# Optimization experiments

Hardware: AMD Instinct MI355X
Metric: run time of the kernel (lower is better)

## Reference

```python
import jax, jax.numpy as jnp
import numpy as np

N, B, DIN, H, D, E = 20000, 2, 128, 4, 64, 320000
NEG_SLOPE = 0.2


def _leaky(x):
    return jnp.where(x >= 0, x, NEG_SLOPE * x)


def setup_inputs() -> dict:
    key = jax.random.key(0)
    k1, k2, k3, k4, k5, k6 = jax.random.split(key, 6)
    feat = jax.random.normal(k1, (N, B, DIN), dtype=jnp.float32)
    # fc weight, xavier-ish scale; stored as (Din, H*D) so projection is feat @ W
    W = jax.random.normal(k2, (DIN, H * D), dtype=jnp.float32) * (1.0 / np.sqrt(DIN))
    attn_l = jax.random.normal(k3, (H, D), dtype=jnp.float32) * 0.1
    attn_r = jax.random.normal(k4, (H, D), dtype=jnp.float32) * 0.1
    src = jax.random.randint(k5, (E,), 0, N, dtype=jnp.int32)
    dst = jax.random.randint(k6, (E,), 0, N, dtype=jnp.int32)
    return {"feat": feat, "W": W, "attn_l": attn_l, "attn_r": attn_r, "src": src, "dst": dst}


def reference(feat, W, attn_l, attn_r, src, dst):
    # feat: (N,B,Din) -> projected features (N,B,H,D)
    ft = (feat @ W).reshape(N, B, H, D)
    # per-node attention logits (N,B,H)
    el = jnp.einsum('nbhd,hd->nbh', ft, attn_l)
    er = jnp.einsum('nbhd,hd->nbh', ft, attn_r)
    # edge logits: u_add_v then LeakyReLU, shape (E,B,H)
    e = _leaky(el[src] + er[dst])
    # edge softmax normalized per destination node (numerically stable)
    emax = jax.ops.segment_max(e, dst, num_segments=N)
    emax = jnp.where(jnp.isfinite(emax), emax, 0.0)  # nodes with no in-edges
    ex = jnp.exp(e - emax[dst])
    denom = jax.ops.segment_sum(ex, dst, num_segments=N)
    a = ex / denom[dst]                               # (E,B,H); denom>0 for every edge's dst
    # u_mul_e messages and sum-aggregation by dst
    m = ft[src] * a[..., None]                        # (E,B,H,D)
    rst = jax.ops.segment_sum(m, dst, num_segments=N)  # (N,B,H,D)
    # module sets self.activation = leaky_relu unconditionally
    return _leaky(rst)
```

## Files before the change

kernel.cpp:

```cpp
#include <hip/hip_runtime.h>
#include <hip/hip_bf16.h>
#include <math.h>


typedef unsigned short ushort;
typedef __attribute__((ext_vector_type(8))) unsigned short ushort8;
typedef __attribute__((ext_vector_type(8))) short short8v;
typedef __attribute__((ext_vector_type(4))) float f32x4;

constexpr int DIN = 128;
constexpr int B   = 2;
constexpr int H   = 4;
constexpr int D   = 64;
constexpr int HD  = H * D;
constexpr int BHD = B * HD;
constexpr int NCOL = 272;
constexpr int PREP_ELEMS  = NCOL * DIN;
constexpr int PREP_BLOCKS = (PREP_ELEMS + 255) / 256;
constexpr int SXS = 72;

__device__ __forceinline__ float leaky(float x) { return x >= 0.f ? x : 0.2f * x; }

__device__ __forceinline__ ushort f2bf(float f) {
    return __builtin_bit_cast(ushort, __float2bfloat16(f));
}
__device__ __forceinline__ float bf2f(ushort v) {
    return __uint_as_float(((unsigned int)v) << 16);
}

__global__ __launch_bounds__(256) void hist_prep_kernel(
    const int* __restrict__ dst, int* __restrict__ deg, int E,
    const float* __restrict__ W, const float* __restrict__ attn_l,
    const float* __restrict__ attn_r, ushort* __restrict__ WT, int histBlocks)
{
    const int t = threadIdx.x;
    const int b = blockIdx.x;
    if (b < histBlocks) {
        int e4 = (b * 256 + t) * 4;
        if (e4 + 3 < E) {
            int4 dd = *(const int4*)(dst + e4);
            atomicAdd(&deg[dd.x], 1); atomicAdd(&deg[dd.y], 1);
            atomicAdd(&deg[dd.z], 1); atomicAdd(&deg[dd.w], 1);
        } else {
            for (int e = e4; e < E; ++e) atomicAdd(&deg[dst[e]], 1);
        }
        return;
    }
    int id = (b - histBlocks) * 256 + t;
    if (id >= PREP_ELEMS) return;
    int c = id >> 7, k = id & 127;
    float v;
    if (c < 256) {
        v = W[k * HD + c];
    } else if (c < 264) {
        int j = c - 256, h = j & 3;
        const float* av = (j < 4 ? attn_l : attn_r) + h * D;
        const float* wp = W + k * HD + h * D;
        float s = 0.f;
        for (int d = 0; d < D; ++d) s = fmaf(wp[d], av[d], s);
        v = s;
    } else {
        v = 0.f;
    }
    WT[c * DIN + k] = f2bf(v);
}

__device__ void scan_body(const int* __restrict__ deg, int* __restrict__ offs,
                          int* __restrict__ cursor, int n)
{
    __shared__ int wcarry[4];
    const int t = threadIdx.x;
    const int lane = t & 63;
    const int wid = t >> 6;
    int carry = 0;
    const int nstripes = (n + 1023) >> 10;
    for (int s = 0; s < nstripes; ++s) {
        const int base = (s << 10) + t * 4;
        int4 d = make_int4(0, 0, 0, 0);
        if (base + 3 < n) {
            d = *(const int4*)(deg + base);
        } else {
            if (base     < n) d.x = deg[base];
            if (base + 1 < n) d.y = deg[base + 1];
            if (base + 2 < n) d.z = deg[base + 2];
        }
        const int sum4 = (d.x + d.y) + (d.z + d.w);
        int inc = sum4;
#pragma unroll
        for (int o = 1; o < 64; o <<= 1) {
            int v = __shfl_up(inc, o, 64);
            if (lane >= o) inc += v;
        }
        if (lane == 63) wcarry[wid] = inc;
        __syncthreads();
        int wpre = carry;
#pragma unroll
        for (int k = 0; k < 4; ++k) if (k < wid) wpre += wcarry[k];
        const int e0 = wpre + inc - sum4;
        int4 ov;
        ov.x = e0; ov.y = e0 + d.x; ov.z = ov.y + d.y; ov.w = ov.z + d.z;
        if (base + 3 < n) {
            *(int4*)(offs + base) = ov;
            *(int4*)(cursor + base) = ov;
        } else {
            if (base     < n) { offs[base]     = ov.x; cursor[base]     = ov.x; }
            if (base + 1 < n) { offs[base + 1] = ov.y; cursor[base + 1] = ov.y; }
            if (base + 2 < n) { offs[base + 2] = ov.z; cursor[base + 2] = ov.z; }
        }
        carry += (wcarry[0] + wcarry[1]) + (wcarry[2] + wcarry[3]);
        __syncthreads();
    }
    if (t == 0) offs[n] = carry;
}

__global__ __launch_bounds__(256) void proj_scan_kernel(
    const float* __restrict__ feat, const ushort* __restrict__ WT,
    ushort* __restrict__ ftb, float* __restrict__ el, float* __restrict__ er,
    const int* __restrict__ deg, int* __restrict__ offs, int* __restrict__ cursor,
    int N, int nTiles)
{
    if ((int)blockIdx.x >= nTiles) {
        scan_body(deg, offs, cursor, N);
        return;
    }
    __shared__ ushort sxp[4][2][16][SXS];
    const int t = threadIdx.x;
    const int w = t >> 6;
    const int lane = t & 63;
    const int lr = lane & 15;
    const int lk = lane >> 4;

    short8v bfrag[4][4];
#pragma unroll
    for (int ct = 0; ct < 4; ++ct) {
        const int col = w * 64 + ct * 16 + lr;
#pragma unroll
        for (int ks = 0; ks < 4; ++ks)
            bfrag[ct][ks] = *(const short8v*)&WT[col * DIN + ks * 32 + lk * 8];
    }
    short8v efrag[4];
#pragma unroll
    for (int ks = 0; ks < 4; ++ks)
        efrag[ks] = *(const short8v*)&WT[(256 + lr) * DIN + ks * 32 + lk * 8];

    const int row0 = blockIdx.x * 64;
    const int rrow = lane >> 2;
    const int seg  = lane & 3;

    auto loadA = [&](int rt, short8v aout[4]) {
        const float* fp = feat + (size_t)(row0 + rt * 16 + lr) * DIN + lk * 8;
#pragma unroll
        for (int ks = 0; ks < 4; ++ks) {
            f32x4 x0 = *(const f32x4*)(fp + ks * 32);
            f32x4 x1 = *(const f32x4*)(fp + ks * 32 + 4);
            short8v v;
            v[0] = (short)f2bf(x0[0]); v[1] = (short)f2bf(x0[1]);
            v[2] = (short)f2bf(x0[2]); v[3] = (short)f2bf(x0[3]);
            v[4] = (short)f2bf(x1[0]); v[5] = (short)f2bf(x1[1]);
            v[6] = (short)f2bf(x1[2]); v[7] = (short)f2bf(x1[3]);
            aout[ks] = v;
        }
    };

    short8v aP[4], aN[4];
    loadA(0, aP);

#pragma unroll
    for (int rt = 0; rt < 4; ++rt) {
        if (rt < 3) loadA(rt + 1, aN);

        f32x4 acc[4] = {{0.f,0.f,0.f,0.f},{0.f,0.f,0.f,0.f},{0.f,0.f,0.f,0.f},{0.f,0.f,0.f,0.f}};
#pragma unroll
        for (int ct = 0; ct < 4; ++ct)
#pragma unroll
            for (int ks = 0; ks < 4; ++ks)
                acc[ct] = __builtin_amdgcn_mfma_f32_16x16x32_bf16(aP[ks], bfrag[ct][ks], acc[ct], 0, 0, 0);

        ushort (* __restrict__ sw)[SXS] = sxp[w][rt & 1];
#pragma unroll
        for (int ct = 0; ct < 4; ++ct)
#pragma unroll
            for (int r = 0; r < 4; ++r)
                sw[lk * 4 + r][ct * 16 + lr] = f2bf(acc[ct][r]);
        __builtin_amdgcn_wave_barrier();
        ushort8 o0 = *(const ushort8*)&sw[rrow][seg * 16];
        ushort8 o1 = *(const ushort8*)&sw[rrow][seg * 16 + 8];
        ushort* gp = ftb + (size_t)(row0 + rt * 16 + rrow) * HD + w * 64 + seg * 16;
        *(ushort8*)gp = o0;
        *(ushort8*)(gp + 8) = o1;

        if (rt == w) {
            f32x4 acce = {0.f, 0.f, 0.f, 0.f};
#pragma unroll
            for (int ks = 0; ks < 4; ++ks)
                acce = __builtin_amdgcn_mfma_f32_16x16x32_bf16(aP[ks], efrag[ks], acce, 0, 0, 0);
#pragma unroll
            for (int r = 0; r < 4; ++r) {
                const int row = row0 + rt * 16 + lk * 4 + r;
                if (lr < 4)       el[row * 4 + lr]       = acce[r];
                else if (lr < 8)  er[row * 4 + (lr - 4)] = acce[r];
            }
        }

#pragma unroll
        for (int ks = 0; ks < 4; ++ks) aP[ks] = aN[ks];
    }
}

__global__ __launch_bounds__(256) void scatter_kernel(
    const int* __restrict__ dst, const int* __restrict__ src,
    int* __restrict__ cursor, int* __restrict__ esrc, int E)
{
    int e4 = (blockIdx.x * 256 + threadIdx.x) * 4;
    if (e4 + 3 < E) {
        int4 dd = *(const int4*)(dst + e4);
        int4 ss = *(const int4*)(src + e4);
        int p0 = atomicAdd(&cursor[dd.x], 1); esrc[p0] = ss.x;
        int p1 = atomicAdd(&cursor[dd.y], 1); esrc[p1] = ss.y;
        int p2 = atomicAdd(&cursor[dd.z], 1); esrc[p2] = ss.z;
        int p3 = atomicAdd(&cursor[dd.w], 1); esrc[p3] = ss.w;
    } else {
        for (int e = e4; e < E; ++e) {
            int pos = atomicAdd(&cursor[dst[e]], 1);
            esrc[pos] = src[e];
        }
    }
}

__global__ __launch_bounds__(256) void agg_kernel(
    const ushort* __restrict__ ftb, const float* __restrict__ el,
    const float* __restrict__ er, const int* __restrict__ offs,
    const int* __restrict__ esrc, float* __restrict__ out, int N)
{
    const int t = threadIdx.x;
    const int n = blockIdx.x * 4 + (t >> 6);
    if (n >= N) return;
    const int lane = t & 63;
    const int bh = lane >> 3;
    const int beg = offs[n];
    const int end = offs[n + 1];

    const float erd = er[n * 8 + bh];
    const ushort8* __restrict__ ftv = (const ushort8*)ftb;

    float acc[8];
#pragma unroll
    for (int j = 0; j < 8; ++j) acc[j] = 0.f;
    float dsum = 0.f;

    int i = beg;
    for (; i + 15 < end; i += 16) {
        int s[16];
#pragma unroll
        for (int u = 0; u < 16; ++u) s[u] = esrc[i + u];
        float w[16];
#pragma unroll
        for (int u = 0; u < 16; ++u) w[u] = __expf(leaky(el[s[u] * 8 + bh] + erd));
        ushort8 v[16];
#pragma unroll
        for (int u = 0; u < 16; ++u) v[u] = ftv[s[u] * 64 + lane];
#pragma unroll
        for (int u = 0; u < 16; ++u) dsum += w[u];
#pragma unroll
        for (int j = 0; j < 8; ++j) {
            float a = acc[j];
#pragma unroll
            for (int u = 0; u < 16; ++u) a = fmaf(w[u], bf2f(v[u][j]), a);
            acc[j] = a;
        }
    }
    for (; i + 3 < end; i += 4) {
        int s[4];
#pragma unroll
        for (int u = 0; u < 4; ++u) s[u] = esrc[i + u];
        float w[4];
#pragma unroll
        for (int u = 0; u < 4; ++u) w[u] = __expf(leaky(el[s[u] * 8 + bh] + erd));
        ushort8 v[4];
#pragma unroll
        for (int u = 0; u < 4; ++u) v[u] = ftv[s[u] * 64 + lane];
#pragma unroll
        for (int u = 0; u < 4; ++u) dsum += w[u];
#pragma unroll
        for (int j = 0; j < 8; ++j) {
            float a = acc[j];
#pragma unroll
            for (int u = 0; u < 4; ++u) a = fmaf(w[u], bf2f(v[u][j]), a);
            acc[j] = a;
        }
    }
    for (; i < end; ++i) {
        int s0 = esrc[i];
        float w0 = __expf(leaky(el[s0 * 8 + bh] + erd));
        ushort8 v0 = ftv[s0 * 64 + lane];
        dsum += w0;
#pragma unroll
        for (int j = 0; j < 8; ++j) acc[j] = fmaf(w0, bf2f(v0[j]), acc[j]);
    }

    const float sc = (end > beg) ? (1.f / dsum) : 0.f;
    float4 o0, o1;
    o0.x = leaky(acc[0] * sc); o0.y = leaky(acc[1] * sc);
    o0.z = leaky(acc[2] * sc); o0.w = leaky(acc[3] * sc);
    o1.x = leaky(acc[4] * sc); o1.y = leaky(acc[5] * sc);
    o1.z = leaky(acc[6] * sc); o1.w = leaky(acc[7] * sc);
    float* op = out + (size_t)n * BHD + lane * 8;
    *(float4*)op = o0;
    *(float4*)(op + 4) = o1;
}

extern "C" void kernel_launch(void* const* d_in, const int* in_sizes, int n_in,
                              void* d_out, int out_size, void* d_ws, size_t ws_size,
                              hipStream_t stream)
{
    const float* feat   = (const float*)d_in[0];
    const float* W      = (const float*)d_in[1];
    const float* attn_l = (const float*)d_in[2];
    const float* attn_r = (const float*)d_in[3];
    const int*   src    = (const int*)d_in[4];
    const int*   dst    = (const int*)d_in[5];
    float* out = (float*)d_out;

    const int N = in_sizes[0] / (B * DIN);
    const int E = in_sizes[4];
    const int R = N * B;
    const int nTiles = R / 64;
    const int histBlocks = (E / 4 + 255) / 256;
    const int edgeBlocks = histBlocks;

    auto align_up = [](size_t x) { return (x + 255) & ~(size_t)255; };
    size_t off = 0;
    char* base = (char*)d_ws;
    ushort* ftb = (ushort*)(base + off); off += align_up((size_t)R * HD * sizeof(ushort));
    float* el   = (float*)(base + off); off += align_up((size_t)R * H * sizeof(float));
    float* er   = (float*)(base + off); off += align_up((size_t)R * H * sizeof(float));
    ushort* WT  = (ushort*)(base + off); off += align_up((size_t)NCOL * DIN * sizeof(ushort));
    int* deg    = (int*)(base + off); off += align_up((size_t)N * sizeof(int));
    int* offs   = (int*)(base + off); off += align_up((size_t)(N + 1) * sizeof(int));
    int* cursor = (int*)(base + off); off += align_up((size_t)N * sizeof(int));
    int* esrc   = (int*)(base + off); off += align_up((size_t)E * sizeof(int));
    (void)ws_size; (void)n_in; (void)out_size;

    hipMemsetAsync(deg, 0, (size_t)N * sizeof(int), stream);

    hist_prep_kernel<<<histBlocks + PREP_BLOCKS, 256, 0, stream>>>(
        dst, deg, E, W, attn_l, attn_r, WT, histBlocks);
    proj_scan_kernel<<<nTiles + 1, 256, 0, stream>>>(
        feat, WT, ftb, el, er, deg, offs, cursor, N, nTiles);
    scatter_kernel<<<edgeBlocks, 256, 0, stream>>>(dst, src, cursor, esrc, E);
    agg_kernel<<<(N + 3) / 4, 256, 0, stream>>>(ftb, el, er, offs, esrc, out, N);
}
```

Baseline: 128.7 us.

## Store projected features per (batch,head) plane and split aggregation by head across blocks

The projection kernel now writes bf16 features as 8 separate (batch,head) planes of N×64 instead of interleaved per node. The aggregation kernel launches 8× more blocks, each handling one (batch,head) slice. Within a wave, 8 lane groups each process a different edge, and the partial sums are combined with xor shuffles. The goal is better locality for the gathers from each plane and more edge-level parallelism per wave, so gather latency is hidden better for low-degree nodes. The cost is that esrc and el are reread once per head, the shuffle reduction adds work, and only one lane group writes the output.

```diff
diff --git a/kernel.cpp b/kernel.cpp
--- a/kernel.cpp
+++ b/kernel.cpp
@@ -115,7 +115,7 @@
 
 __global__ __launch_bounds__(256) void proj_scan_kernel(
     const float* __restrict__ feat, const ushort* __restrict__ WT,
-    ushort* __restrict__ ftb, float* __restrict__ el, float* __restrict__ er,
+    ushort* __restrict__ ftt, float* __restrict__ el, float* __restrict__ er,
     const int* __restrict__ deg, int* __restrict__ offs, int* __restrict__ cursor,
     int N, int nTiles)
 {
@@ -185,7 +185,10 @@
         __builtin_amdgcn_wave_barrier();
         ushort8 o0 = *(const ushort8*)&sw[rrow][seg * 16];
         ushort8 o1 = *(const ushort8*)&sw[rrow][seg * 16 + 8];
-        ushort* gp = ftb + (size_t)(row0 + rt * 16 + rrow) * HD + w * 64 + seg * 16;
+        const int row = row0 + rt * 16 + rrow;
+        const int nn = row >> 1;
+        const int bb = row & 1;
+        ushort* gp = ftt + ((size_t)(bb * 4 + w) * N + nn) * 64 + seg * 16;
         *(ushort8*)gp = o0;
         *(ushort8*)(gp + 8) = o1;
 
@@ -196,9 +199,9 @@
                 acce = __builtin_amdgcn_mfma_f32_16x16x32_bf16(aP[ks], efrag[ks], acce, 0, 0, 0);
 #pragma unroll
             for (int r = 0; r < 4; ++r) {
-                const int row = row0 + rt * 16 + lk * 4 + r;
-                if (lr < 4)       el[row * 4 + lr]       = acce[r];
-                else if (lr < 8)  er[row * 4 + (lr - 4)] = acce[r];
+                const int row2 = row0 + rt * 16 + lk * 4 + r;
+                if (lr < 4)       el[row2 * 4 + lr]       = acce[r];
+                else if (lr < 8)  er[row2 * 4 + (lr - 4)] = acce[r];
             }
         }
 
@@ -228,85 +231,69 @@
 }
 
 __global__ __launch_bounds__(256) void agg_kernel(
-    const ushort* __restrict__ ftb, const float* __restrict__ el,
+    const ushort* __restrict__ ftt, const float* __restrict__ el,
     const float* __restrict__ er, const int* __restrict__ offs,
     const int* __restrict__ esrc, float* __restrict__ out, int N)
 {
     const int t = threadIdx.x;
-    const int n = blockIdx.x * 4 + (t >> 6);
+    const int bh = blockIdx.x & 7;
+    const int n  = (blockIdx.x >> 3) * 4 + (t >> 6);
     if (n >= N) return;
     const int lane = t & 63;
-    const int bh = lane >> 3;
+    const int g  = lane >> 3;
+    const int d8 = lane & 7;
     const int beg = offs[n];
     const int end = offs[n + 1];
-
     const float erd = er[n * 8 + bh];
-    const ushort8* __restrict__ ftv = (const ushort8*)ftb;
+    const ushort8* __restrict__ fv = (const ushort8*)(ftt + (size_t)bh * N * 64);
 
     float acc[8];
 #pragma unroll
     for (int j = 0; j < 8; ++j) acc[j] = 0.f;
     float dsum = 0.f;
 
-    int i = beg;
-    for (; i + 15 < end; i += 16) {
-        int s[16];
-#pragma unroll
-        for (int u = 0; u < 16; ++u) s[u] = esrc[i + u];
-        float w[16];
-#pragma unroll
-        for (int u = 0; u < 16; ++u) w[u] = __expf(leaky(el[s[u] * 8 + bh] + erd));
-        ushort8 v[16];
-#pragma unroll
-        for (int u = 0; u < 16; ++u) v[u] = ftv[s[u] * 64 + lane];
-#pragma unroll
-        for (int u = 0; u < 16; ++u) dsum += w[u];
-#pragma unroll
-        for (int j = 0; j < 8; ++j) {
-            float a = acc[j];
-#pragma unroll
-            for (int u = 0; u < 16; ++u) a = fmaf(w[u], bf2f(v[u][j]), a);
-            acc[j] = a;
-        }
-    }
-    for (; i + 3 < end; i += 4) {
-        int s[4];
-#pragma unroll
-        for (int u = 0; u < 4; ++u) s[u] = esrc[i + u];
-        float w[4];
-#pragma unroll
-        for (int u = 0; u < 4; ++u) w[u] = __expf(leaky(el[s[u] * 8 + bh] + erd));
-        ushort8 v[4];
-#pragma unroll
-        for (int u = 0; u < 4; ++u) v[u] = ftv[s[u] * 64 + lane];
-#pragma unroll
-        for (int u = 0; u < 4; ++u) dsum += w[u];
-#pragma unroll
-        for (int j = 0; j < 8; ++j) {
-            float a = acc[j];
-#pragma unroll
-            for (int u = 0; u < 4; ++u) a = fmaf(w[u], bf2f(v[u][j]), a);
-            acc[j] = a;
-        }
-    }
-    for (; i < end; ++i) {
+    int i = beg + g;
+    for (; i + 8 < end; i += 16) {
         int s0 = esrc[i];
-        float w0 = __expf(leaky(el[s0 * 8 + bh] + erd));
-        ushort8 v0 = ftv[s0 * 64 + lane];
+        int s1 = esrc[i + 8];
+        float x0 = el[(size_t)s0 * 8 + bh];
+        float x1 = el[(size_t)s1 * 8 + bh];
+        ushort8 v0 = fv[(size_t)s0 * 8 + d8];
+        ushort8 v1 = fv[(size_t)s1 * 8 + d8];
+        float w0 = __expf(leaky(x0 + erd));
+        float w1 = __expf(leaky(x1 + erd));
+        dsum += w0 + w1;
+#pragma unroll
+        for (int j = 0; j < 8; ++j)
+            acc[j] += w0 * bf2f(v0[j]) + w1 * bf2f(v1[j]);
+    }
+    if (i < end) {
+        int s0 = esrc[i];
+        float w0 = __expf(leaky(el[(size_t)s0 * 8 + bh] + erd));
+        ushort8 v0 = fv[(size_t)s0 * 8 + d8];
         dsum += w0;
 #pragma unroll
         for (int j = 0; j < 8; ++j) acc[j] = fmaf(w0, bf2f(v0[j]), acc[j]);
     }
 
-    const float sc = (end > beg) ? (1.f / dsum) : 0.f;
-    float4 o0, o1;
-    o0.x = leaky(acc[0] * sc); o0.y = leaky(acc[1] * sc);
-    o0.z = leaky(acc[2] * sc); o0.w = leaky(acc[3] * sc);
-    o1.x = leaky(acc[4] * sc); o1.y = leaky(acc[5] * sc);
-    o1.z = leaky(acc[6] * sc); o1.w = leaky(acc[7] * sc);
-    float* op = out + (size_t)n * BHD + lane * 8;
-    *(float4*)op = o0;
-    *(float4*)(op + 4) = o1;
+#pragma unroll
+    for (int o = 8; o < 64; o <<= 1) {
+        dsum += __shfl_xor(dsum, o, 64);
+#pragma unroll
+        for (int j = 0; j < 8; ++j) acc[j] += __shfl_xor(acc[j], o, 64);
+    }
+
+    if (g == 0) {
+        const float sc = (end > beg) ? (1.f / dsum) : 0.f;
+        float4 o0, o1;
+        o0.x = leaky(acc[0] * sc); o0.y = leaky(acc[1] * sc);
+        o0.z = leaky(acc[2] * sc); o0.w = leaky(acc[3] * sc);
+        o1.x = leaky(acc[4] * sc); o1.y = leaky(acc[5] * sc);
+        o1.z = leaky(acc[6] * sc); o1.w = leaky(acc[7] * sc);
+        float* op = out + (size_t)n * BHD + bh * 64 + d8 * 8;
+        *(float4*)op = o0;
+        *(float4*)(op + 4) = o1;
+    }
 }
 
 extern "C" void kernel_launch(void* const* d_in, const int* in_sizes, int n_in,
@@ -331,7 +318,7 @@
     auto align_up = [](size_t x) { return (x + 255) & ~(size_t)255; };
     size_t off = 0;
     char* base = (char*)d_ws;
-    ushort* ftb = (ushort*)(base + off); off += align_up((size_t)R * HD * sizeof(ushort));
+    ushort* ftt = (ushort*)(base + off); off += align_up((size_t)R * HD * sizeof(ushort));
     float* el   = (float*)(base + off); off += align_up((size_t)R * H * sizeof(float));
     float* er   = (float*)(base + off); off += align_up((size_t)R * H * sizeof(float));
     ushort* WT  = (ushort*)(base + off); off += align_up((size_t)NCOL * DIN * sizeof(ushort));
@@ -346,7 +333,7 @@
     hist_prep_kernel<<<histBlocks + PREP_BLOCKS, 256, 0, stream>>>(
         dst, deg, E, W, attn_l, attn_r, WT, histBlocks);
     proj_scan_kernel<<<nTiles + 1, 256, 0, stream>>>(
-        feat, WT, ftb, el, er, deg, offs, cursor, N, nTiles);
+        feat, WT, ftt, el, er, deg, offs, cursor, N, nTiles);
     scatter_kernel<<<edgeBlocks, 256, 0, stream>>>(dst, src, cursor, esrc, E);
-    agg_kernel<<<(N + 3) / 4, 256, 0, stream>>>(ftb, el, er, offs, esrc, out, N);
-}
+    agg_kernel<<<8 * ((N + 3) / 4), 256, 0, stream>>>(ftt, el, er, offs, esrc, out, N);
+}
```

Result: slower. 133.9 us (+4.1%).
